# Performance work log

Measured on AMD Instinct MI355X. Metric: run time of the kernel, lower is better.

The kernel has to match this reference:

```python
import jax, jax.numpy as jnp
import numpy as np
from jax import lax

NEG = -1e9  # effective -inf, safe for fp32 and for gradients


def asg_loss(inputs, transitions, targets):
    """ASG criterion (wav2letter / gtn_applications semantics).

    inputs:      [B, T, N] emissions (log scores)
    transitions: [N+1, N]; transitions[0, i] = start score of class i,
                 transitions[i+1, j] = score of transition j -> i
    targets:     [B, L] int class ids (already replabel-packed + garbage-interleaved)
    Returns mean over batch of (logZ - forced_align_score) / L.
    """
    B, T, N = inputs.shape
    L = targets.shape[1]
    init = transitions[0]      # [N]
    trans = transitions[1:]    # [N, N], trans[i, j]: j -> i

    # ---- denominator: free recursion over all label sequences ----
    alpha0 = inputs[:, 0, :] + init  # [B, N]
    emis_t = jnp.swapaxes(inputs, 0, 1)  # [T, B, N]

    def den_step(alpha, e_t):
        # alpha[b, j] -> new alpha[b, i] = e_t[b, i] + LSE_j(alpha[b, j] + trans[i, j])
        a = jax.nn.logsumexp(alpha[:, None, :] + trans[None, :, :], axis=-1) + e_t
        return a, None

    alphaT, _ = lax.scan(den_step, alpha0, emis_t[1:])
    logZ = jax.nn.logsumexp(alphaT, axis=-1)  # [B]

    # ---- numerator: forced-alignment graph (self-loop or advance) ----
    # emissions gathered at target labels: [B, T, L]
    emis_y = jnp.take_along_axis(inputs, jnp.broadcast_to(targets[:, None, :], (B, T, L)), axis=2)
    stay_w = trans[targets, targets]                      # [B, L]   y_s -> y_s
    adv_w = trans[targets[:, 1:], targets[:, :-1]]        # [B, L-1] y_{s-1} -> y_s

    beta0 = jnp.full((B, L), NEG, dtype=inputs.dtype)
    beta0 = beta0.at[:, 0].set(init[targets[:, 0]] + emis_y[:, 0, 0])
    emis_y_t = jnp.swapaxes(emis_y, 0, 1)  # [T, B, L]

    def num_step(beta, e_t):
        stay = beta + stay_w
        adv = jnp.concatenate(
            [jnp.full((B, 1), NEG, dtype=beta.dtype), beta[:, :-1] + adv_w], axis=1)
        b = jnp.logaddexp(stay, adv) + e_t
        return b, None

    betaT, _ = lax.scan(num_step, beta0, emis_y_t[1:])
    target_score = betaT[:, -1]  # must end having consumed all L labels

    # reduction = 'mean': scale each sample by 1/len(target), then batch mean
    return jnp.mean((logZ - target_score) / L)


def setup_inputs() -> dict:
    key = jax.random.key(0)
    k1, k2, k3 = jax.random.split(key, 3)
    B, T, N, L = 128, 4000, 64, 101
    inputs = jax.random.normal(k1, (B, T, N), dtype=jnp.float32)
    transitions = jax.random.normal(k2, (N + 1, N), dtype=jnp.float32) * 0.1
    targets = jax.random.randint(k3, (B, L), 0, N, dtype=jnp.int64)
    return {"inputs": inputs, "transitions": transitions, "targets": targets}


def reference(inputs, transitions, targets):
    return asg_loss(inputs, transitions, targets)
```

## Files before the change

kernel.cpp:

```cpp
#include <hip/hip_runtime.h>


#define TT 4000
#define NN 64
#define LL 101
#define NSEG 32

static constexpr float L2E  = 1.44269504088896340736f;
static constexpr float LN2F = 0.69314718055994530942f;
static constexpr float NEG2 = -1.0e30f;

#define WS_X    0
#define WS_NF   4096
#define WS_HB   18432
#define WS_LOSS 32768

#if defined(__has_builtin)
#if __has_builtin(__builtin_amdgcn_mfma_f32_16x16x16bf16_1k)
#define BF16MM 1
#endif
#if __has_builtin(__builtin_amdgcn_exp2f)
#define FEXP2(x) __builtin_amdgcn_exp2f(x)
#endif
#if __has_builtin(__builtin_amdgcn_logf)
#define FLOG2(x) __builtin_amdgcn_logf(x)
#endif
#endif
#ifndef FEXP2
#define FEXP2(x) exp2f(x)
#endif
#ifndef FLOG2
#define FLOG2(x) log2f(x)
#endif

typedef float f32x4 __attribute__((ext_vector_type(4)));
typedef short s16x4 __attribute__((ext_vector_type(4)));
typedef _Float16 h4 __attribute__((ext_vector_type(4)));

__device__ __forceinline__ unsigned cvt2(float a, float b) {
#ifdef BF16MM
  const unsigned ua = __builtin_bit_cast(unsigned, a);
  const unsigned ub = __builtin_bit_cast(unsigned, b);
  const unsigned ra = (ua + 0x7FFFu + ((ua >> 16) & 1u)) >> 16;
  const unsigned rb = (ub + 0x7FFFu + ((ub >> 16) & 1u)) >> 16;
  return ra | (rb << 16);
#else
  return __builtin_bit_cast(unsigned,
      __builtin_amdgcn_cvt_pkrtz(fminf(a, 3.0e4f), fminf(b, 3.0e4f)));
#endif
}

__device__ __forceinline__ f32x4 MM(uint2 a, uint2 b, f32x4 c) {
#ifdef BF16MM
  return __builtin_amdgcn_mfma_f32_16x16x16bf16_1k(
      __builtin_bit_cast(s16x4, a), __builtin_bit_cast(s16x4, b), c, 0, 0, 0);
#else
  return __builtin_amdgcn_mfma_f32_16x16x16f16(
      __builtin_bit_cast(h4, a), __builtin_bit_cast(h4, b), c, 0, 0, 0);
#endif
}

template<int CTRL>
__device__ __forceinline__ float dppf(float x) {
  return __builtin_bit_cast(float, __builtin_amdgcn_update_dpp(
      0, __builtin_bit_cast(int, x), CTRL, 0xf, 0xf, true));
}

template<int DIR>
__device__ __forceinline__ void num_chain(const float* __restrict__ em,
                                          const float* __restrict__ TR,
                                          const int* __restrict__ Y,
                                          float* __restrict__ ws,
                                          const int b, const int l)
{
  const bool v0 = (2 * l     <= 100);
  const bool v1 = (2 * l + 1 <= 100);
  const int k0 = v0 ? 2 * l     : 100;
  const int k1 = v1 ? 2 * l + 1 : 100;
  const int y0 = Y[b * LL + k0];
  const int y1 = Y[b * LL + k1];
  const float SW0 = v0 ? FEXP2(TR[(y0 + 1) * NN + y0] * L2E) : 0.f;
  const float SW1 = v1 ? FEXP2(TR[(y1 + 1) * NN + y1] * L2E) : 0.f;
  float WLOC, WRECV, B0, B1, C;
  bool recvok;
  if (DIR == 0) {
    WLOC = v1 ? FEXP2(TR[(y1 + 1) * NN + y0] * L2E) : 0.f;
    const int ym0 = Y[b * LL + (k0 > 0 ? k0 - 1 : 0)];
    recvok = v0 && (l > 0);
    WRECV = recvok ? FEXP2(TR[(y0 + 1) * NN + ym0] * L2E) : 0.f;
    B0 = (l == 0) ? 1.f : 0.f;
    B1 = 0.f;
    C  = (l == 0) ? (TR[y0] + em[y0]) * L2E : 0.f;
  } else {
    WLOC = v1 ? FEXP2(TR[(y1 + 1) * NN + y0] * L2E) : 0.f;
    const int kp = (2 * l + 2 <= 100) ? 2 * l + 2 : 100;
    const int yp1 = Y[b * LL + kp];
    recvok = (2 * l + 2 <= 100);
    WRECV = recvok ? FEXP2(TR[(yp1 + 1) * NN + y1] * L2E) : 0.f;
    B0 = (l == 50) ? 1.f : 0.f;
    B1 = 0.f;
    C  = (l == 50) ? em[(size_t)(TT - 1) * NN + y0] * L2E : 0.f;
  }

#define TROW(t) ((size_t)((DIR == 0) ? (t) : (TT - 1 - (t))) * NN)

  float ca[8], cb[8], na[8], nb[8];
#pragma unroll
  for (int k = 0; k < 8; ++k) {
    ca[k] = em[TROW(1 + k) + y0];
    cb[k] = em[TROW(1 + k) + y1];
  }
#pragma unroll
  for (int k = 0; k < 8; ++k) {
    na[k] = em[TROW(9 + k) + y0];
    nb[k] = em[TROW(9 + k) + y1];
  }

  float ADJ = 0.f;

#define RESCALE()                                                              \
  {                                                                            \
    const float v = B0 + B1;                                                   \
    const int bits = __builtin_bit_cast(int, v);                               \
    const int m = (v > 0.f) ? ((bits >> 23) & 255) - 127 : 0;                  \
    const float sc = __builtin_bit_cast(float, (127 - m) << 23);               \
    B0 *= sc; B1 *= sc; C += (float)m;                                         \
    const float Cn = dppf<(DIR == 0) ? 0x138 : 0x130>(C);                      \
    const float dC = fminf(fmaxf(Cn - C, -120.f), 120.f);                      \
    ADJ = recvok ? FEXP2(dC) * WRECV : 0.f;                                    \
  }

#define NSTEP(EA, EB)                                                          \
  {                                                                            \
    const float E0 = FEXP2((EA) * L2E);                                        \
    const float E1 = FEXP2((EB) * L2E);                                        \
    if (DIR == 0) {                                                            \
      const float NB = dppf<0x138>(B1);                                        \
      const float t0 = fmaf(NB, ADJ, B0 * SW0);                                \
      const float t1 = fmaf(B0, WLOC, B1 * SW1);                               \
      B0 = t0 * E0; B1 = t1 * E1;                                              \
    } else {                                                                   \
      const float NB = dppf<0x130>(B0);                                        \
      const float t1 = fmaf(NB, ADJ, B1 * SW1);                                \
      const float t0 = fmaf(B1, WLOC, B0 * SW0);                               \
      B0 = t0 * E0; B1 = t1 * E1;                                              \
    }                                                                          \
  }

  for (int ep = 0; ep < 249; ++ep) {
    RESCALE();
    float pa[8], pb[8];
#pragma unroll
    for (int k = 0; k < 8; ++k) {
      int t = 17 + 8 * ep + k;
      t = (t < 1999) ? t : 1999;
      pa[k] = em[TROW(t) + y0];
      pb[k] = em[TROW(t) + y1];
    }
#pragma unroll
    for (int k = 0; k < 8; ++k) NSTEP(ca[k], cb[k]);
#pragma unroll
    for (int k = 0; k < 8; ++k) { ca[k] = na[k]; cb[k] = nb[k];
                                  na[k] = pa[k]; nb[k] = pb[k]; }
  }
  RESCALE();
#pragma unroll
  for (int k = 0; k < 7; ++k) NSTEP(ca[k], cb[k]);

#undef NSTEP
#undef RESCALE
#undef TROW

  const float o0 = (B0 > 1e-37f) ? C + FLOG2(B0) : NEG2;
  const float o1 = (B1 > 1e-37f) ? C + FLOG2(B1) : NEG2;
  const int base = (DIR ? WS_HB : WS_NF) + b * 112;
  if (v0) ws[base + 2 * l]     = o0;
  if (v1) ws[base + 2 * l + 1] = o1;
}

__global__ __launch_bounds__(128) void asg_main(
    const float* __restrict__ E, const float* __restrict__ TR,
    const int* __restrict__ Y, float* __restrict__ ws)
{
  const int bid  = blockIdx.x;
  const int w    = threadIdx.x >> 6;
  const int lane = threadIdx.x & 63;
  const int b    = bid >> 1;
  const float* em = E + (size_t)b * TT * NN;

  if (w == 0) {
    const int h = bid & 1;
    const int c = lane & 15, g = lane >> 4;
    const int j = h * 16 + c;

    uint2 Af[4][4];
#pragma unroll
    for (int rt = 0; rt < 4; ++rt)
#pragma unroll
      for (int kt = 0; kt < 4; ++kt) {
        const float* tr = TR + (size_t)(16 * rt + c + 1) * NN + 16 * kt + 4 * g;
        const float w0 = FEXP2(tr[0] * L2E), w1 = FEXP2(tr[1] * L2E);
        const float w2 = FEXP2(tr[2] * L2E), w3 = FEXP2(tr[3] * L2E);
        Af[rt][kt].x = cvt2(w0, w1);
        Af[rt][kt].y = cvt2(w2, w3);
      }

    f32x4 P[4];
#pragma unroll
    for (int rt = 0; rt < 4; ++rt)
#pragma unroll
      for (int e = 0; e < 4; ++e) {
        const int row = 16 * rt + 4 * g + e;
        P[rt][e] = (j == 0) ? FEXP2((em[row] + TR[row]) * L2E) : 1.0f;
      }

    float Csum = 0.f, snap31 = 0.f;
    const float* ebase = em + (size_t)(124 * j + 1) * NN + 4 * g;

#define COLSUM(dst) { float t_ =                                               \
      (P[0].x + P[0].y + P[0].z + P[0].w) + (P[1].x + P[1].y + P[1].z + P[1].w)\
    + (P[2].x + P[2].y + P[2].z + P[2].w) + (P[3].x + P[3].y + P[3].z + P[3].w);\
    t_ += __shfl_xor(t_, 16); t_ += __shfl_xor(t_, 32);                        \
    (dst) = fmaxf(t_, 1e-30f); }

#define RENORM() { float cs_; COLSUM(cs_);                                     \
    const int mb_ = ((__builtin_bit_cast(int, cs_) >> 23) & 255) - 127;        \
    const float sc_ = __builtin_bit_cast(float, (127 - mb_) << 23);            \
    P[0] *= sc_; P[1] *= sc_; P[2] *= sc_; P[3] *= sc_;                        \
    Csum += (float)mb_; }

#define ELOAD(D, s_) { const int se_ = (s_) < 154 ? (s_) : 154;                \
    const f32x4* p_ = (const f32x4*)(ebase + (size_t)se_ * NN);                \
    D[0] = p_[0]; D[1] = p_[4]; D[2] = p_[8]; D[3] = p_[12]; }

#define STEP(M)                                                                \
    {                                                                          \
      uint2 Bf[4];                                                             \
      _Pragma("unroll") for (int kt = 0; kt < 4; ++kt) {                       \
        Bf[kt].x = cvt2(P[kt].x, P[kt].y);                                     \
        Bf[kt].y = cvt2(P[kt].z, P[kt].w);                                     \
      }                                                                        \
      _Pragma("unroll") for (int rt = 0; rt < 4; ++rt) {                       \
        f32x4 acc = {0.f, 0.f, 0.f, 0.f};                                      \
        acc = MM(Af[rt][0], Bf[0], acc);                                       \
        acc = MM(Af[rt][1], Bf[1], acc);                                       \
        acc = MM(Af[rt][2], Bf[2], acc);                                       \
        acc = MM(Af[rt][3], Bf[3], acc);                                       \
        _Pragma("unroll") for (int e = 0; e < 4; ++e)                          \
          P[rt][e] = fminf(fmaxf(                                              \
              acc[e] * FEXP2(fmaf(M[rt][e], L2E, -6.7f)), 1e-20f), 1e25f);     \
      }                                                                        \
    }

#define SUB(Ebuf, ss)                                                          \
    { f32x4 T_[4] = {Ebuf[0], Ebuf[1], Ebuf[2], Ebuf[3]};                      \
      ELOAD(Ebuf, (ss) + 4);                                                   \
      STEP(T_);                                                                \
      if ((ss) == 30) { float cs2_; COLSUM(cs2_);                              \
                        snap31 = Csum + FLOG2(cs2_) + 6.7f * 31.f; }           \
      if (((ss) & 7) == 7) RENORM(); }

    f32x4 E0[4], E1[4], E2[4], E3[4];
    ELOAD(E0, 0); ELOAD(E1, 1); ELOAD(E2, 2); ELOAD(E3, 3);

    for (int it = 0; it < 38; ++it) {
      const int s = 4 * it;
      SUB(E0, s); SUB(E1, s + 1); SUB(E2, s + 2); SUB(E3, s + 3);
    }
    { f32x4 T_[4] = {E0[0], E0[1], E0[2], E0[3]}; STEP(T_); }
    { f32x4 T_[4] = {E1[0], E1[1], E1[2], E1[3]}; STEP(T_); }
    { f32x4 T_[4] = {E2[0], E2[1], E2[2], E2[3]}; STEP(T_); }

    float csf; COLSUM(csf);
    const float fin = Csum + FLOG2(csf) + 6.7f * 155.f;
    const float X = fin - ((j == 0) ? 0.f : snap31);
    if (lane < 16) ws[WS_X + b * NSEG + (h * 16 + lane)] = X;

#undef SUB
#undef STEP
#undef ELOAD
#undef RENORM
#undef COLSUM

  } else {
    const int dir = bid & 1;
    if (dir == 0) num_chain<0>(em, TR, Y, ws, b, lane);
    else          num_chain<1>(em, TR, Y, ws, b, lane);
  }
}

__global__ __launch_bounds__(128) void asg_combine(
    const float* __restrict__ TR, const int* __restrict__ Y,
    const float* __restrict__ ws, float* __restrict__ lossv)
{
  const int b = blockIdx.x;
  const int tid = threadIdx.x;
  __shared__ float sN[LL], sH[LL], red[128];
  __shared__ float sLogZ;

  if (tid == 0) {
    float z = 0.f;
    for (int s = 0; s < NSEG; ++s) z += ws[WS_X + b * NSEG + s];
    sLogZ = z;
  }
  if (tid < LL) { sN[tid] = ws[WS_NF + b * 112 + tid]; sH[tid] = ws[WS_HB + b * 112 + tid]; }
  __syncthreads();

  float val2 = -3.0e38f;
  if (tid < LL) {
    const int l = tid;
    const int y = Y[b * LL + l];
    const float s1 = sN[l] + TR[(y + 1) * NN + y] * L2E;
    float s2 = NEG2;
    if (l > 0) {
      const int ymm = Y[b * LL + l - 1];
      s2 = sN[l - 1] + TR[(y + 1) * NN + ymm] * L2E;
    }
    const float m = fmaxf(s1, s2);
    val2 = m + log2f(exp2f(s1 - m) + exp2f(s2 - m)) + sH[l];
  }
  red[tid] = val2;
  __syncthreads();
  if (tid == 0) {
    float m = red[0];
    for (int k = 1; k < LL; ++k) m = fmaxf(m, red[k]);
    float s = 0.f;
    for (int k = 0; k < LL; ++k) s += exp2f(red[k] - m);
    const float tgt2 = m + log2f(s);
    lossv[b] = (sLogZ - tgt2) * LN2F / (float)LL;
  }
}

__global__ __launch_bounds__(64) void asg_reduce(const float* __restrict__ lossv,
                                                 float* __restrict__ out)
{
  const int tid = threadIdx.x;
  float v = lossv[tid] + lossv[tid + 64];
  for (int off = 32; off; off >>= 1) v += __shfl_xor(v, off);
  if (tid == 0) out[0] = v * (1.0f / 128.0f);
}

extern "C" void kernel_launch(void* const* d_in, const int* in_sizes, int n_in,
                              void* d_out, int out_size, void* d_ws, size_t ws_size,
                              hipStream_t stream) {
  const float* E  = (const float*)d_in[0];
  const float* TR = (const float*)d_in[1];
  const int*   Y  = (const int*)d_in[2];
  float* out = (float*)d_out;
  float* ws  = (float*)d_ws;
  float* lossv = ws + WS_LOSS;

  asg_main<<<dim3(256), dim3(128), 0, stream>>>(E, TR, Y, ws);
  asg_combine<<<dim3(128), dim3(128), 0, stream>>>(TR, Y, ws, lossv);
  asg_reduce<<<dim3(1), dim3(64), 0, stream>>>(lossv, out);
}
```

Before: 127.1 us.

## Coalesce numerator emission loads with shuffles and deepen prefetch pipelines

```diff
diff --git a/kernel.cpp b/kernel.cpp
--- a/kernel.cpp
+++ b/kernel.cpp
@@ -104,71 +104,95 @@
 
 #define TROW(t) ((size_t)((DIR == 0) ? (t) : (TT - 1 - (t))) * NN)
 
-  float ca[8], cb[8], na[8], nb[8];
-#pragma unroll
-  for (int k = 0; k < 8; ++k) {
-    ca[k] = em[TROW(1 + k) + y0];
-    cb[k] = em[TROW(1 + k) + y1];
-  }
-#pragma unroll
-  for (int k = 0; k < 8; ++k) {
-    na[k] = em[TROW(9 + k) + y0];
-    nb[k] = em[TROW(9 + k) + y1];
-  }
-
+  float RA[16], RB[16], RC[16];
+  float PC0[16], PC1[16];
+  float PN0[16], PN1[16];
   float ADJ = 0.f;
+
+#define ISSUE(R, e)                                                            \
+  { _Pragma("unroll") for (int k_ = 0; k_ < 16; ++k_) {                        \
+      int t_ = 1 + 16 * (e) + k_; t_ = (t_ < 1999) ? t_ : 1999;                \
+      R[k_] = em[TROW(t_) + l]; } }
+
+#define PROC(P0, P1, R)                                                        \
+  { _Pragma("unroll") for (int k_ = 0; k_ < 16; ++k_) {                        \
+      const float r_ = R[k_];                                                  \
+      const float a_ = __shfl(r_, y0);                                         \
+      const float b_ = __shfl(r_, y1);                                         \
+      P0[k_] = FEXP2(a_ * L2E);                                                \
+      P1[k_] = FEXP2(b_ * L2E); } }
+
+#define COPYP()                                                                \
+  { _Pragma("unroll") for (int k_ = 0; k_ < 16; ++k_) {                        \
+      PC0[k_] = PN0[k_]; PC1[k_] = PN1[k_]; } }
 
 #define RESCALE()                                                              \
   {                                                                            \
-    const float v = B0 + B1;                                                   \
-    const int bits = __builtin_bit_cast(int, v);                               \
-    const int m = (v > 0.f) ? ((bits >> 23) & 255) - 127 : 0;                  \
-    const float sc = __builtin_bit_cast(float, (127 - m) << 23);               \
-    B0 *= sc; B1 *= sc; C += (float)m;                                         \
-    const float Cn = dppf<(DIR == 0) ? 0x138 : 0x130>(C);                      \
-    const float dC = fminf(fmaxf(Cn - C, -120.f), 120.f);                      \
-    ADJ = recvok ? FEXP2(dC) * WRECV : 0.f;                                    \
-  }
-
-#define NSTEP(EA, EB)                                                          \
+    const float v_ = B0 + B1;                                                  \
+    const int bits_ = __builtin_bit_cast(int, v_);                             \
+    const int m_ = (v_ > 0.f) ? ((bits_ >> 23) & 255) - 127 : 0;               \
+    const float sc_ = __builtin_bit_cast(float, (127 - m_) << 23);             \
+    B0 *= sc_; B1 *= sc_; C += (float)m_;                                      \
+    const float Cn_ = dppf<(DIR == 0) ? 0x138 : 0x130>(C);                     \
+    const float dC_ = fminf(fmaxf(Cn_ - C, -120.f), 120.f);                    \
+    ADJ = recvok ? FEXP2(dC_) * WRECV : 0.f;                                   \
+  }
+
+#define NSTEP2(E0v, E1v)                                                       \
   {                                                                            \
-    const float E0 = FEXP2((EA) * L2E);                                        \
-    const float E1 = FEXP2((EB) * L2E);                                        \
     if (DIR == 0) {                                                            \
       const float NB = dppf<0x138>(B1);                                        \
       const float t0 = fmaf(NB, ADJ, B0 * SW0);                                \
       const float t1 = fmaf(B0, WLOC, B1 * SW1);                               \
-      B0 = t0 * E0; B1 = t1 * E1;                                              \
+      B0 = t0 * (E0v); B1 = t1 * (E1v);                                        \
     } else {                                                                   \
       const float NB = dppf<0x130>(B0);                                        \
       const float t1 = fmaf(NB, ADJ, B1 * SW1);                                \
       const float t0 = fmaf(B1, WLOC, B0 * SW0);                               \
-      B0 = t0 * E0; B1 = t1 * E1;                                              \
+      B0 = t0 * (E0v); B1 = t1 * (E1v);                                        \
     }                                                                          \
   }
 
-  for (int ep = 0; ep < 249; ++ep) {
-    RESCALE();
-    float pa[8], pb[8];
-#pragma unroll
-    for (int k = 0; k < 8; ++k) {
-      int t = 17 + 8 * ep + k;
-      t = (t < 1999) ? t : 1999;
-      pa[k] = em[TROW(t) + y0];
-      pb[k] = em[TROW(t) + y1];
-    }
-#pragma unroll
-    for (int k = 0; k < 8; ++k) NSTEP(ca[k], cb[k]);
-#pragma unroll
-    for (int k = 0; k < 8; ++k) { ca[k] = na[k]; cb[k] = nb[k];
-                                  na[k] = pa[k]; nb[k] = pb[k]; }
-  }
+#define RUN16()                                                                \
+  { RESCALE();                                                                 \
+    _Pragma("unroll") for (int k_ = 0; k_ < 8; ++k_)                           \
+      NSTEP2(PC0[k_], PC1[k_]);                                                \
+    RESCALE();                                                                 \
+    _Pragma("unroll") for (int k_ = 8; k_ < 16; ++k_)                          \
+      NSTEP2(PC0[k_], PC1[k_]); }
+
+#define PHASE(e, Rslot)                                                        \
+  { RUN16();                                                                   \
+    COPYP();                                                                   \
+    PROC(PN0, PN1, Rslot);                                                     \
+    ISSUE(Rslot, (e) + 5); }
+
+  ISSUE(RA, 0); ISSUE(RB, 1); ISSUE(RC, 2);
+  PROC(PC0, PC1, RA);  ISSUE(RA, 3);
+  PROC(PN0, PN1, RB);  ISSUE(RB, 4);
+
+  for (int s = 0; s < 41; ++s) {
+    const int e = 3 * s;
+    PHASE(e,     RC);
+    PHASE(e + 1, RA);
+    PHASE(e + 2, RB);
+  }
+  RUN16();
+  COPYP();
   RESCALE();
 #pragma unroll
-  for (int k = 0; k < 7; ++k) NSTEP(ca[k], cb[k]);
-
-#undef NSTEP
+  for (int k_ = 0; k_ < 8; ++k_) NSTEP2(PC0[k_], PC1[k_]);
+  RESCALE();
+#pragma unroll
+  for (int k_ = 8; k_ < 15; ++k_) NSTEP2(PC0[k_], PC1[k_]);
+
+#undef PHASE
+#undef RUN16
+#undef NSTEP2
 #undef RESCALE
+#undef COPYP
+#undef PROC
+#undef ISSUE
 #undef TROW
 
   const float o0 = (B0 > 1e-37f) ? C + FLOG2(B0) : NEG2;
@@ -252,24 +276,28 @@
       }                                                                        \
     }
 
-#define SUB(Ebuf, ss)                                                          \
+#define SUB(Ebuf, ss, kr)                                                      \
     { f32x4 T_[4] = {Ebuf[0], Ebuf[1], Ebuf[2], Ebuf[3]};                      \
-      ELOAD(Ebuf, (ss) + 4);                                                   \
+      ELOAD(Ebuf, (ss) + 6);                                                   \
       STEP(T_);                                                                \
       if ((ss) == 30) { float cs2_; COLSUM(cs2_);                              \
                         snap31 = Csum + FLOG2(cs2_) + 6.7f * 31.f; }           \
-      if (((ss) & 7) == 7) RENORM(); }
-
-    f32x4 E0[4], E1[4], E2[4], E3[4];
-    ELOAD(E0, 0); ELOAD(E1, 1); ELOAD(E2, 2); ELOAD(E3, 3);
-
-    for (int it = 0; it < 38; ++it) {
-      const int s = 4 * it;
-      SUB(E0, s); SUB(E1, s + 1); SUB(E2, s + 2); SUB(E3, s + 3);
+      if ((kr) == 5) RENORM(); }
+
+    f32x4 E0[4], E1[4], E2[4], E3[4], E4[4], E5[4];
+    ELOAD(E0, 0); ELOAD(E1, 1); ELOAD(E2, 2);
+    ELOAD(E3, 3); ELOAD(E4, 4); ELOAD(E5, 5);
+
+    for (int it = 0; it < 25; ++it) {
+      const int s = 6 * it;
+      SUB(E0, s, 0);     SUB(E1, s + 1, 1); SUB(E2, s + 2, 2);
+      SUB(E3, s + 3, 3); SUB(E4, s + 4, 4); SUB(E5, s + 5, 5);
     }
     { f32x4 T_[4] = {E0[0], E0[1], E0[2], E0[3]}; STEP(T_); }
     { f32x4 T_[4] = {E1[0], E1[1], E1[2], E1[3]}; STEP(T_); }
     { f32x4 T_[4] = {E2[0], E2[1], E2[2], E2[3]}; STEP(T_); }
+    { f32x4 T_[4] = {E3[0], E3[1], E3[2], E3[3]}; STEP(T_); }
+    { f32x4 T_[4] = {E4[0], E4[1], E4[2], E4[3]}; STEP(T_); }
 
     float csf; COLSUM(csf);
     const float fin = Csum + FLOG2(csf) + 6.7f * 155.f;
```

New measurement: 131.2 us. +3.2%, slower.
